# Performance work log

Hardware: AMD Instinct MI355X
Metric: run time of the kernel (lower is better)

Reference implementation:

```python
import jax, jax.numpy as jnp
import numpy as np

L, B, E, H = 2048, 4, 1024, 8
D1 = 2 * E  # expand_ratio * embed_dim, already divisible by H
EPS = 1e-8


def setup_inputs() -> dict:
    key = jax.random.key(0)
    ks = jax.random.split(key, 12)
    std = 0.02
    return {
        "query": jax.random.normal(ks[0], (L, B, E), jnp.float32),
        "key": jax.random.normal(ks[1], (L, B, E), jnp.float32),
        "value": jax.random.normal(ks[2], (L, B, E), jnp.float32),
        "u_w": jax.random.normal(ks[3], (D1, E), jnp.float32) * std,
        "u_b": jax.random.normal(ks[4], (D1,), jnp.float32) * std,
        "v_w": jax.random.normal(ks[5], (D1, E), jnp.float32) * std,
        "v_b": jax.random.normal(ks[6], (D1,), jnp.float32) * std,
        "o_w": jax.random.normal(ks[7], (E, D1), jnp.float32) * std,
        "o_b": jax.random.normal(ks[8], (E,), jnp.float32) * std,
        # Toeplitz relative-position coefficients: t_0 (zero), t_1..t_{n-1} (pos), t_{-1}..t_{-(n-1)} (neg)
        "pos": jax.random.normal(ks[9], (H, L - 1), jnp.float32) * std,
        "zero": jax.random.normal(ks[10], (H, 1), jnp.float32) * std,
        "neg": jax.random.normal(ks[11], (H, L - 1), jnp.float32) * std,
    }


def _toeplitz_mix(v, pos, zero, neg):
    # v: (b, h, n, d). y_i = sum_j t_{i-j} v_j via circular conv of length 2n.
    b, h, n, d = v.shape
    m = 2 * n
    # a[0]=t_0, a[1:n]=t_1..t_{n-1}, a[n]=0 (unused), a[n+1:2n]=t_{-(n-1)}..t_{-1}
    a = jnp.concatenate([zero, pos[:, : n - 1], jnp.zeros((h, 1), v.dtype), neg[:, : n - 1][:, ::-1]], axis=-1)
    af = jnp.fft.rfft(a, n=m, axis=-1)            # (h, n+1)
    vf = jnp.fft.rfft(v, n=m, axis=-2)            # (b, h, n+1, d)
    y = jnp.fft.irfft(af[None, :, :, None] * vf, n=m, axis=-2)
    return y[:, :, :n, :]


def reference(query, key, value, u_w, u_b, v_w, v_b, o_w, o_b, pos, zero, neg):
    n, b, e = query.shape
    # SimpleRMSNorm: x / (||x||_2 / sqrt(d) + eps)
    rms = jnp.linalg.norm(query, axis=-1, keepdims=True) * (e ** -0.5)
    x = query / (rms + EPS)
    u = jax.nn.silu(jnp.einsum("nbe,fe->nbf", x, u_w) + u_b)   # (n, b, d1)
    v = jax.nn.silu(jnp.einsum("nbe,fe->nbf", x, v_w) + v_b)   # (n, b, d1)
    hd = v.shape[-1] // H
    vh = v.reshape(n, b, H, hd).transpose(1, 2, 0, 3)          # (b, h, n, d)
    y = _toeplitz_mix(vh, pos, zero, neg)                      # (b, h, n, d)
    y = y.transpose(2, 0, 1, 3).reshape(n, b, H * hd)          # (n, b, d1)
    out = u * y
    return jnp.einsum("nbf,ef->nbe", out, o_w) + o_b + query
```

## Files before the change

kernel.cpp:

```cpp
#include <hip/hip_runtime.h>
#include <math.h>

typedef unsigned short u16;
typedef __bf16 bf16x8 __attribute__((ext_vector_type(8)));
typedef float f32x4 __attribute__((ext_vector_type(4)));

#define LSEQ 2048
#define NB   4
#define NE   1024
#define NHEAD 8
#define ND1  2048
#define NHD  256
#define NM   8192
#define CRP  4104

__device__ __forceinline__ u16 f2bf(float f) {
  unsigned u = __float_as_uint(f);
  u += 0x7FFFu + ((u >> 16) & 1u);
  return (u16)(u >> 16);
}
__device__ __forceinline__ float bf2f(u16 h) {
  return __uint_as_float(((unsigned)h) << 16);
}
__device__ __forceinline__ unsigned mulbf2(unsigned y2, unsigned u2) {
  float ylo = bf2f((u16)(y2 & 0xFFFF)), yhi = bf2f((u16)(y2 >> 16));
  float ulo = bf2f((u16)(u2 & 0xFFFF)), uhi = bf2f((u16)(u2 >> 16));
  return (unsigned)f2bf(ylo * ulo) | ((unsigned)f2bf(yhi * uhi) << 16);
}

__device__ __forceinline__ void gl_lds16(const u16* g, u16* l) {
  __builtin_amdgcn_global_load_lds(
      (const __attribute__((address_space(1))) void*)g,
      (__attribute__((address_space(3))) void*)l, 16, 0, 0);
}

__global__ __launch_bounds__(256) void prep_kernel(
    const float* __restrict__ uw, const float* __restrict__ vw,
    const float* __restrict__ ow, u16* __restrict__ uwb, u16* __restrict__ vwb,
    u16* __restrict__ owb, const float* __restrict__ pos,
    const float* __restrict__ zero, const float* __restrict__ neg,
    u16* __restrict__ cr8) {
  int bx = blockIdx.x;
  if (bx < 6144) {
    const float* s = bx < 2048 ? uw : (bx < 4096 ? vw : ow);
    u16* d = bx < 2048 ? uwb : (bx < 4096 ? vwb : owb);
    int i = (bx & 2047) * 256 + threadIdx.x;
    float4 v = ((const float4*)s)[i];
    ushort4 o;
    o.x = f2bf(v.x); o.y = f2bf(v.y); o.z = f2bf(v.z); o.w = f2bf(v.w);
    ((ushort4*)d)[i] = o;
  } else {
    int bb = bx - 6144;
    int h = bb >> 3, sh = bb & 7;
    u16* out = cr8 + (size_t)bb * CRP;
    for (int m = threadIdx.x; m < CRP; m += 256) {
      int mm = m + sh;
      float val = 0.f;
      if (mm <= 4094) {
        int t = 2047 - mm;
        if (t == 0)      val = zero[h];
        else if (t > 0)  val = pos[h * (LSEQ - 1) + t - 1];
        else             val = neg[h * (LSEQ - 1) + (-t) - 1];
      }
      out[m] = f2bf(val);
    }
  }
}

__global__ __launch_bounds__(256) void rmsnorm_kernel(const float* __restrict__ q,
                                                      u16* __restrict__ x) {
  int row = blockIdx.x;
  float4 v = ((const float4*)(q + (size_t)row * NE))[threadIdx.x];
  float ss = v.x * v.x + v.y * v.y + v.z * v.z + v.w * v.w;
  #pragma unroll
  for (int off = 32; off > 0; off >>= 1) ss += __shfl_down(ss, off, 64);
  __shared__ float wss[4];
  int wave = threadIdx.x >> 6, lane = threadIdx.x & 63;
  if (lane == 0) wss[wave] = ss;
  __syncthreads();
  float tot = wss[0] + wss[1] + wss[2] + wss[3];
  float scale = 1.f / (sqrtf(tot) * 0.03125f + 1e-8f);
  ushort4 o;
  o.x = f2bf(v.x * scale); o.y = f2bf(v.y * scale);
  o.z = f2bf(v.z * scale); o.w = f2bf(v.w * scale);
  ((ushort4*)(x + (size_t)row * NE))[threadIdx.x] = o;
}

__global__ __launch_bounds__(256) void transpose_v(const u16* __restrict__ v,
                                                   u16* __restrict__ vT) {
  __shared__ u16 s[64 * 68];
  int j0 = blockIdx.x * 64, d0 = blockIdx.y * 64;
  int h = blockIdx.z >> 2, b = blockIdx.z & 3;
  #pragma unroll
  for (int it = 0; it < 4; ++it) {
    int idx = it * 256 + threadIdx.x;
    int r = idx >> 4, c4 = idx & 15;
    *(ushort4*)&s[r * 68 + c4 * 4] =
        *(const ushort4*)&v[((size_t)(j0 + r) * NB + b) * ND1 + h * NHD + d0 + c4 * 4];
  }
  __syncthreads();
  #pragma unroll
  for (int it = 0; it < 4; ++it) {
    int idx = it * 256 + threadIdx.x;
    int cc = idx >> 4, jq = idx & 15;
    ushort4 o;
    o.x = s[(jq * 4 + 0) * 68 + cc];
    o.y = s[(jq * 4 + 1) * 68 + cc];
    o.z = s[(jq * 4 + 2) * 68 + cc];
    o.w = s[(jq * 4 + 3) * 68 + cc];
    *(ushort4*)&vT[((size_t)h * (NB * NHD) + b * NHD + d0 + cc) * LSEQ + j0 + jq * 4] = o;
  }
}


__device__ __forceinline__ bf16x8 ldsfrag(const u16* buf, int rr, int q) {
  return *(const bf16x8*)(buf + rr * 64 + ((q ^ (rr & 7)) * 8));
}

template <int MODE>
__device__ __forceinline__ void stage_Ah(const u16* A, const u16* Acr, int Ksz,
                                         int i0, int kt, int half, u16* dstbuf,
                                         int tid) {
  int wave = tid >> 6;
  #pragma unroll
  for (int it = 0; it < 2; ++it) {
    int vv = it * 512 + tid;
    int r = vv >> 3, c8 = vv & 7, c8s = c8 ^ (r & 7);
    int row = i0 + half * 128 + r;
    const u16* src;
    if (MODE != 1) {
      src = A + (size_t)row * Ksz + kt * 64 + c8s * 8;
    } else {
      int p = 2047 - row + kt * 64;
      int s = p & 7, qq = p - s;
      src = Acr + (size_t)s * CRP + qq + c8s * 8;
    }
    gl_lds16(src, dstbuf + half * 8192 + (it * 512 + wave * 64) * 8);
  }
}

__device__ __forceinline__ void stage_Bh(const u16* B, int Ksz, int n0, int kt,
                                         int half, u16* dstbuf, int tid) {
  int wave = tid >> 6;
  #pragma unroll
  for (int it = 0; it < 2; ++it) {
    int vv = it * 512 + tid;
    int r = vv >> 3, c8 = vv & 7, c8s = c8 ^ (r & 7);
    gl_lds16(B + (size_t)(n0 + half * 128 + r) * Ksz + kt * 64 + c8s * 8,
             dstbuf + half * 8192 + (it * 512 + wave * 64) * 8);
  }
}

#define PHASE_MID()                                        \
  __builtin_amdgcn_s_barrier();                            \
  asm volatile("s_waitcnt lgkmcnt(0)" ::: "memory");       \
  __builtin_amdgcn_sched_barrier(0);                       \
  __builtin_amdgcn_s_setprio(1);

#define PHASE_END()                                        \
  __builtin_amdgcn_s_setprio(0);                           \
  __builtin_amdgcn_s_barrier();                            \
  __builtin_amdgcn_sched_barrier(0);

template <int MODE>
__global__ __launch_bounds__(512, 2) void gemm256(
    const u16* __restrict__ A, const u16* __restrict__ Bw0,
    const u16* __restrict__ Bw1, const float* __restrict__ bias0,
    const float* __restrict__ bias1, u16* __restrict__ C0,
    u16* __restrict__ C1, int Msz, int Nsz, int Ksz) {
  extern __shared__ __align__(16) u16 lds[];
  u16* As = lds;
  u16* Ws = lds + 32768;

  const int tid = threadIdx.x;
  const int lane = tid & 63, wave = tid >> 6;
  const int wr = (wave >> 2) * 128, wc = (wave & 3) * 64;
  const int lr = lane & 15, lq = lane >> 4;
  const int i0 = blockIdx.y * 256, n0 = blockIdx.x * 256;

  const u16* Bh;
  const u16* Acr = A;
  const float* bias = bias0;
  u16* Cp = C0;
  if (MODE == 0) {
    Bh = blockIdx.z ? Bw1 : Bw0;
    bias = blockIdx.z ? bias1 : bias0;
    Cp = blockIdx.z ? C1 : C0;
  } else {
    Bh  = Bw0 + (size_t)blockIdx.z * Nsz * Ksz;
    Acr = A + (size_t)blockIdx.z * 8 * CRP;
  }
  const int nkt = Ksz >> 6;

  f32x4 acc[8][4];
  #pragma unroll
  for (int a = 0; a < 8; ++a)
    #pragma unroll
    for (int b = 0; b < 4; ++b) acc[a][b] = (f32x4){0.f, 0.f, 0.f, 0.f};

  stage_Ah<MODE>(A, Acr, Ksz, i0, 0, 0, As, tid);
  stage_Ah<MODE>(A, Acr, Ksz, i0, 0, 1, As, tid);
  stage_Bh(Bh, Ksz, n0, 0, 0, Ws, tid);
  stage_Bh(Bh, Ksz, n0, 0, 1, Ws, tid);
  stage_Bh(Bh, Ksz, n0, 1, 0, Ws + 16384, tid);
  stage_Bh(Bh, Ksz, n0, 1, 1, Ws + 16384, tid);
  asm volatile("s_waitcnt vmcnt(4)" ::: "memory");
  __builtin_amdgcn_s_barrier();
  __builtin_amdgcn_sched_barrier(0);

  for (int tt = 0; tt < nkt; ++tt) {
    const int cur = tt & 1;
    const u16* Ab = As + cur * 16384;
    const u16* Wb = Ws + cur * 16384;
    u16* An = As + (cur ^ 1) * 16384;
    u16* Wn = Ws + cur * 16384;

    bf16x8 a[4][2], b[4][2];

    #pragma unroll
    for (int rt = 0; rt < 4; ++rt) {
      int ar = wr + rt * 16 + lr;
      a[rt][0] = ldsfrag(Ab, ar, lq);
      a[rt][1] = ldsfrag(Ab, ar, 4 + lq);
    }
    #pragma unroll
    for (int ct = 0; ct < 4; ++ct) {
      int br = wc + ct * 16 + lr;
      b[ct][0] = ldsfrag(Wb, br, lq);
      b[ct][1] = ldsfrag(Wb, br, 4 + lq);
    }
    if (tt + 1 < nkt) {
      stage_Ah<MODE>(A, Acr, Ksz, i0, tt + 1, 0, An, tid);
      stage_Ah<MODE>(A, Acr, Ksz, i0, tt + 1, 1, An, tid);
    }
    PHASE_MID();
    #pragma unroll
    for (int rt = 0; rt < 4; ++rt)
      #pragma unroll
      for (int ct = 0; ct < 4; ++ct) {
        acc[rt][ct] = __builtin_amdgcn_mfma_f32_16x16x32_bf16(a[rt][0], b[ct][0], acc[rt][ct], 0, 0, 0);
        acc[rt][ct] = __builtin_amdgcn_mfma_f32_16x16x32_bf16(a[rt][1], b[ct][1], acc[rt][ct], 0, 0, 0);
      }
    PHASE_END();

    #pragma unroll
    for (int rt = 0; rt < 4; ++rt) {
      int ar = wr + (rt + 4) * 16 + lr;
      a[rt][0] = ldsfrag(Ab, ar, lq);
      a[rt][1] = ldsfrag(Ab, ar, 4 + lq);
    }
    if (tt + 2 < nkt) {
      stage_Bh(Bh, Ksz, n0, tt + 2, 0, Wn, tid);
      stage_Bh(Bh, Ksz, n0, tt + 2, 1, Wn, tid);
    }
    if (tt == nkt - 2) { asm volatile("s_waitcnt vmcnt(0)" ::: "memory"); }
    else               { asm volatile("s_waitcnt vmcnt(4)" ::: "memory"); }
    PHASE_MID();
    #pragma unroll
    for (int rt = 0; rt < 4; ++rt)
      #pragma unroll
      for (int ct = 0; ct < 4; ++ct) {
        acc[rt + 4][ct] = __builtin_amdgcn_mfma_f32_16x16x32_bf16(a[rt][0], b[ct][0], acc[rt + 4][ct], 0, 0, 0);
        acc[rt + 4][ct] = __builtin_amdgcn_mfma_f32_16x16x32_bf16(a[rt][1], b[ct][1], acc[rt + 4][ct], 0, 0, 0);
      }
    PHASE_END();
  }

  __syncthreads();
  u16* zl = lds;
  #pragma unroll
  for (int rt = 0; rt < 8; ++rt) {
    #pragma unroll
    for (int ct = 0; ct < 4; ++ct) {
      int col_l = wc + ct * 16 + lr;
      #pragma unroll
      for (int reg = 0; reg < 4; ++reg) {
        int row_l = wr + rt * 16 + lq * 4 + reg;
        float yv = acc[rt][ct][reg];
        if (MODE == 0) {
          float t = yv + bias[n0 + col_l];
          yv = t / (1.f + __expf(-t));
        }
        zl[row_l * 256 + (col_l ^ (((row_l >> 2) & 3) << 4))] = f2bf(yv);
      }
    }
  }
  __syncthreads();
  #pragma unroll
  for (int k = 0; k < 16; ++k) {
    int cc = k * 512 + tid;
    int row_l = cc >> 5, c8 = cc & 31;
    int colbase = c8 * 8;
    int swz = colbase ^ (((row_l >> 2) & 3) << 4);
    uint4 y4 = *(uint4*)&zl[row_l * 256 + swz];
    if (MODE == 0) {
      *(uint4*)&Cp[(size_t)(i0 + row_l) * Nsz + n0 + colbase] = y4;
    } else {
      size_t ui = ((size_t)(i0 + row_l) * NB + blockIdx.x) * ND1 +
                  (size_t)blockIdx.z * NHD + colbase;
      uint4 u4 = *(const uint4*)&Cp[ui];
      uint4 o;
      o.x = mulbf2(y4.x, u4.x); o.y = mulbf2(y4.y, u4.y);
      o.z = mulbf2(y4.z, u4.z); o.w = mulbf2(y4.w, u4.w);
      *(uint4*)&Cp[ui] = o;
    }
  }
}

__global__ __launch_bounds__(256) void gemm_out(
    const u16* __restrict__ A, const u16* __restrict__ Bw,
    const float* __restrict__ bias, const float* __restrict__ resid,
    float* __restrict__ Cf, int Nsz, int Ksz) {
  __shared__ __align__(16) u16 As[128 * 64];
  __shared__ __align__(16) u16 Ws[128 * 64];

  const int tid = threadIdx.x;
  const int lane = tid & 63, wave = tid >> 6;
  const int wr = (wave >> 1) * 64, wc = (wave & 1) * 64;
  const int lr = lane & 15, lq = lane >> 4;
  const int i0 = blockIdx.y * 128, n0 = blockIdx.x * 128;

  f32x4 acc[4][4];
  #pragma unroll
  for (int a = 0; a < 4; ++a)
    #pragma unroll
    for (int b = 0; b < 4; ++b) acc[a][b] = (f32x4){0.f, 0.f, 0.f, 0.f};

  const int nkt = Ksz >> 6;
  for (int kt = 0; kt < nkt; ++kt) {
    #pragma unroll
    for (int it = 0; it < 4; ++it) {
      int vv = tid + 256 * it;
      int r = vv >> 3, c8 = vv & 7;
      int c8s = c8 ^ (r & 7);
      gl_lds16(A + (size_t)(i0 + r) * Ksz + kt * 64 + c8s * 8,
               &As[(size_t)(wave * 64 + it * 256) * 8]);
    }
    #pragma unroll
    for (int it = 0; it < 4; ++it) {
      int vv = tid + 256 * it;
      int r = vv >> 3, c8 = vv & 7;
      int c8s = c8 ^ (r & 7);
      gl_lds16(Bw + (size_t)(n0 + r) * Ksz + kt * 64 + c8s * 8,
               &Ws[(size_t)(wave * 64 + it * 256) * 8]);
    }
    __syncthreads();
    #pragma unroll
    for (int ks = 0; ks < 2; ++ks) {
      bf16x8 af[4], bfr[4];
      #pragma unroll
      for (int rt = 0; rt < 4; ++rt) {
        int ar = wr + rt * 16 + lr;
        int cq = (ks * 4 + lq) ^ (ar & 7);
        af[rt] = *(const bf16x8*)&As[ar * 64 + cq * 8];
      }
      #pragma unroll
      for (int ct = 0; ct < 4; ++ct) {
        int br = wc + ct * 16 + lr;
        int cq = (ks * 4 + lq) ^ (br & 7);
        bfr[ct] = *(const bf16x8*)&Ws[br * 64 + cq * 8];
      }
      #pragma unroll
      for (int rt = 0; rt < 4; ++rt)
        #pragma unroll
        for (int ct = 0; ct < 4; ++ct)
          acc[rt][ct] = __builtin_amdgcn_mfma_f32_16x16x32_bf16(
              af[rt], bfr[ct], acc[rt][ct], 0, 0, 0);
    }
    __syncthreads();
  }

  #pragma unroll
  for (int rt = 0; rt < 4; ++rt) {
    #pragma unroll
    for (int ct = 0; ct < 4; ++ct) {
      int col = n0 + wc + ct * 16 + lr;
      #pragma unroll
      for (int reg = 0; reg < 4; ++reg) {
        int row = i0 + wr + rt * 16 + lq * 4 + reg;
        size_t oi = (size_t)row * Nsz + col;
        Cf[oi] = acc[rt][ct][reg] + bias[col] + resid[oi];
      }
    }
  }
}

extern "C" void kernel_launch(void* const* d_in, const int* in_sizes, int n_in,
                              void* d_out, int out_size, void* d_ws, size_t ws_size,
                              hipStream_t stream) {
  const float* q    = (const float*)d_in[0];
  const float* uw   = (const float*)d_in[3];
  const float* ub   = (const float*)d_in[4];
  const float* vw   = (const float*)d_in[5];
  const float* vb   = (const float*)d_in[6];
  const float* ow   = (const float*)d_in[7];
  const float* ob   = (const float*)d_in[8];
  const float* pos  = (const float*)d_in[9];
  const float* zero = (const float*)d_in[10];
  const float* neg  = (const float*)d_in[11];
  float* out = (float*)d_out;

  char* ws = (char*)d_ws;
  u16* x   = (u16*)(ws + 0);
  u16* uwb = (u16*)(ws + 16777216);
  u16* vwb = (u16*)(ws + 20971520);
  u16* owb = (u16*)(ws + 25165824);
  u16* u   = (u16*)(ws + 29360128);
  u16* v   = (u16*)(ws + 62914560);
  u16* vT  = (u16*)(ws + 96468992);
  u16* cr8 = (u16*)(ws + 130023424);

  hipFuncSetAttribute((const void*)gemm256<0>,
                      hipFuncAttributeMaxDynamicSharedMemorySize, 131072);
  hipFuncSetAttribute((const void*)gemm256<1>,
                      hipFuncAttributeMaxDynamicSharedMemorySize, 131072);

  prep_kernel<<<6208, 256, 0, stream>>>(uw, vw, ow, uwb, vwb, owb,
                                        pos, zero, neg, cr8);
  rmsnorm_kernel<<<NM, 256, 0, stream>>>(q, x);

  gemm256<0><<<dim3(8, 32, 2), 512, 131072, stream>>>(x, uwb, vwb, ub, vb, u, v,
                                                      NM, ND1, NE);
  transpose_v<<<dim3(32, 4, 32), 256, 0, stream>>>(v, vT);
  gemm256<1><<<dim3(4, 8, 8), 512, 131072, stream>>>(cr8, vT, nullptr, nullptr,
                                                     nullptr, u, nullptr,
                                                     LSEQ, NB * NHD, LSEQ);
  gemm_out<<<dim3(8, 64, 1), 256, 0, stream>>>(u, owb, ob, q, out, NE, ND1);
}
```

Measured before the change: 368.5 us.

## Fuse v transpose into projection GEMM epilogue, triple-buffer A, remap workgroups

Removes the separate transpose_v kernel: the v-projection blocks of the first GEMM now write their SiLU output transposed through LDS straight into the head-major vT layout. This drops one full write and read of the v intermediate and one kernel launch. The A operand staging goes from double to triple buffering with a deeper prefetch, raising dynamic LDS from 128 KB to 160 KB per block, which may lower the number of resident blocks per CU. Both GEMM kernels also remap workgroup IDs with a stride-8 interleave, intended to spread blocks across XCDs for better L2 locality.

```diff
diff --git a/kernel.cpp b/kernel.cpp
--- a/kernel.cpp
+++ b/kernel.cpp
@@ -86,32 +86,6 @@
   ((ushort4*)(x + (size_t)row * NE))[threadIdx.x] = o;
 }
 
-__global__ __launch_bounds__(256) void transpose_v(const u16* __restrict__ v,
-                                                   u16* __restrict__ vT) {
-  __shared__ u16 s[64 * 68];
-  int j0 = blockIdx.x * 64, d0 = blockIdx.y * 64;
-  int h = blockIdx.z >> 2, b = blockIdx.z & 3;
-  #pragma unroll
-  for (int it = 0; it < 4; ++it) {
-    int idx = it * 256 + threadIdx.x;
-    int r = idx >> 4, c4 = idx & 15;
-    *(ushort4*)&s[r * 68 + c4 * 4] =
-        *(const ushort4*)&v[((size_t)(j0 + r) * NB + b) * ND1 + h * NHD + d0 + c4 * 4];
-  }
-  __syncthreads();
-  #pragma unroll
-  for (int it = 0; it < 4; ++it) {
-    int idx = it * 256 + threadIdx.x;
-    int cc = idx >> 4, jq = idx & 15;
-    ushort4 o;
-    o.x = s[(jq * 4 + 0) * 68 + cc];
-    o.y = s[(jq * 4 + 1) * 68 + cc];
-    o.z = s[(jq * 4 + 2) * 68 + cc];
-    o.w = s[(jq * 4 + 3) * 68 + cc];
-    *(ushort4*)&vT[((size_t)h * (NB * NHD) + b * NHD + d0 + cc) * LSEQ + j0 + jq * 4] = o;
-  }
-}
-
 
 __device__ __forceinline__ bf16x8 ldsfrag(const u16* buf, int rr, int q) {
   return *(const bf16x8*)(buf + rr * 64 + ((q ^ (rr & 7)) * 8));
@@ -170,25 +144,32 @@
     u16* __restrict__ C1, int Msz, int Nsz, int Ksz) {
   extern __shared__ __align__(16) u16 lds[];
   u16* As = lds;
-  u16* Ws = lds + 32768;
+  u16* Ws = lds + 49152;
+
+  unsigned gx = gridDim.x, gy = gridDim.y;
+  unsigned nwg = gx * gy * gridDim.z;
+  unsigned lin = blockIdx.x + gx * (blockIdx.y + gy * blockIdx.z);
+  unsigned w = (lin & 7) * (nwg >> 3) + (lin >> 3);
+  unsigned bx = w % gx, rest = w / gx;
+  unsigned by = rest % gy, bz = rest / gy;
 
   const int tid = threadIdx.x;
   const int lane = tid & 63, wave = tid >> 6;
   const int wr = (wave >> 2) * 128, wc = (wave & 3) * 64;
   const int lr = lane & 15, lq = lane >> 4;
-  const int i0 = blockIdx.y * 256, n0 = blockIdx.x * 256;
+  const int i0 = by * 256, n0 = bx * 256;
 
   const u16* Bh;
   const u16* Acr = A;
   const float* bias = bias0;
   u16* Cp = C0;
   if (MODE == 0) {
-    Bh = blockIdx.z ? Bw1 : Bw0;
-    bias = blockIdx.z ? bias1 : bias0;
-    Cp = blockIdx.z ? C1 : C0;
+    Bh = bz ? Bw1 : Bw0;
+    bias = bz ? bias1 : bias0;
+    Cp = bz ? C1 : C0;
   } else {
-    Bh  = Bw0 + (size_t)blockIdx.z * Nsz * Ksz;
-    Acr = A + (size_t)blockIdx.z * 8 * CRP;
+    Bh  = Bw0 + (size_t)bz * Nsz * Ksz;
+    Acr = A + (size_t)bz * 8 * CRP;
   }
   const int nkt = Ksz >> 6;
 
@@ -202,18 +183,19 @@
   stage_Ah<MODE>(A, Acr, Ksz, i0, 0, 1, As, tid);
   stage_Bh(Bh, Ksz, n0, 0, 0, Ws, tid);
   stage_Bh(Bh, Ksz, n0, 0, 1, Ws, tid);
+  stage_Ah<MODE>(A, Acr, Ksz, i0, 1, 0, As + 16384, tid);
+  stage_Ah<MODE>(A, Acr, Ksz, i0, 1, 1, As + 16384, tid);
   stage_Bh(Bh, Ksz, n0, 1, 0, Ws + 16384, tid);
   stage_Bh(Bh, Ksz, n0, 1, 1, Ws + 16384, tid);
-  asm volatile("s_waitcnt vmcnt(4)" ::: "memory");
+  asm volatile("s_waitcnt vmcnt(8)" ::: "memory");
   __builtin_amdgcn_s_barrier();
   __builtin_amdgcn_sched_barrier(0);
 
   for (int tt = 0; tt < nkt; ++tt) {
-    const int cur = tt & 1;
-    const u16* Ab = As + cur * 16384;
-    const u16* Wb = Ws + cur * 16384;
-    u16* An = As + (cur ^ 1) * 16384;
-    u16* Wn = Ws + cur * 16384;
+    const u16* Ab = As + (tt % 3) * 16384;
+    const u16* Wb = Ws + (tt & 1) * 16384;
+    u16* An = As + ((tt + 2) % 3) * 16384;
+    u16* Wn = Ws + (tt & 1) * 16384;
 
     bf16x8 a[4][2], b[4][2];
 
@@ -229,9 +211,9 @@
       b[ct][0] = ldsfrag(Wb, br, lq);
       b[ct][1] = ldsfrag(Wb, br, 4 + lq);
     }
-    if (tt + 1 < nkt) {
-      stage_Ah<MODE>(A, Acr, Ksz, i0, tt + 1, 0, An, tid);
-      stage_Ah<MODE>(A, Acr, Ksz, i0, tt + 1, 1, An, tid);
+    if (tt + 2 < nkt) {
+      stage_Ah<MODE>(A, Acr, Ksz, i0, tt + 2, 0, An, tid);
+      stage_Ah<MODE>(A, Acr, Ksz, i0, tt + 2, 1, An, tid);
     }
     PHASE_MID();
     #pragma unroll
@@ -254,7 +236,7 @@
       stage_Bh(Bh, Ksz, n0, tt + 2, 1, Wn, tid);
     }
     if (tt == nkt - 2) { asm volatile("s_waitcnt vmcnt(0)" ::: "memory"); }
-    else               { asm volatile("s_waitcnt vmcnt(4)" ::: "memory"); }
+    else               { asm volatile("s_waitcnt vmcnt(8)" ::: "memory"); }
     PHASE_MID();
     #pragma unroll
     for (int rt = 0; rt < 4; ++rt)
@@ -267,6 +249,38 @@
   }
 
   __syncthreads();
+  if (MODE == 0 && bz == 1) {
+    u16* zt = lds;
+    #pragma unroll
+    for (int rt = 0; rt < 8; ++rt) {
+      #pragma unroll
+      for (int ct = 0; ct < 4; ++ct) {
+        int col_l = wc + ct * 16 + lr;
+        #pragma unroll
+        for (int reg = 0; reg < 4; ++reg) {
+          int row_l = wr + rt * 16 + lq * 4 + reg;
+          float t = acc[rt][ct][reg] + bias[n0 + col_l];
+          t = t / (1.f + __expf(-t));
+          zt[col_l * 256 + (row_l ^ (row_l >> 4) ^ ((col_l & 15) << 2))] = f2bf(t);
+        }
+      }
+    }
+    __syncthreads();
+    int j0 = by * 64;
+    #pragma unroll
+    for (int it2 = 0; it2 < 32; ++it2) {
+      int g = it2 * 512 + tid;
+      int jq = g & 15, b2 = (g >> 4) & 3, d = g >> 6;
+      int rl0 = 16 * jq + b2, sd = (d & 15) << 2;
+      ushort4 o;
+      o.x = zt[d * 256 + ((rl0 + 0)  ^ ((rl0 + 0)  >> 4) ^ sd)];
+      o.y = zt[d * 256 + ((rl0 + 4)  ^ ((rl0 + 4)  >> 4) ^ sd)];
+      o.z = zt[d * 256 + ((rl0 + 8)  ^ ((rl0 + 8)  >> 4) ^ sd)];
+      o.w = zt[d * 256 + ((rl0 + 12) ^ ((rl0 + 12) >> 4) ^ sd)];
+      *(ushort4*)&Cp[((size_t)bx * (NB * NHD) + b2 * NHD + d) * LSEQ + j0 + jq * 4] = o;
+    }
+    return;
+  }
   u16* zl = lds;
   #pragma unroll
   for (int rt = 0; rt < 8; ++rt) {
@@ -296,8 +310,8 @@
     if (MODE == 0) {
       *(uint4*)&Cp[(size_t)(i0 + row_l) * Nsz + n0 + colbase] = y4;
     } else {
-      size_t ui = ((size_t)(i0 + row_l) * NB + blockIdx.x) * ND1 +
-                  (size_t)blockIdx.z * NHD + colbase;
+      size_t ui = ((size_t)(i0 + row_l) * NB + bx) * ND1 +
+                  (size_t)bz * NHD + colbase;
       uint4 u4 = *(const uint4*)&Cp[ui];
       uint4 o;
       o.x = mulbf2(y4.x, u4.x); o.y = mulbf2(y4.y, u4.y);
@@ -314,11 +328,17 @@
   __shared__ __align__(16) u16 As[128 * 64];
   __shared__ __align__(16) u16 Ws[128 * 64];
 
+  unsigned gx = gridDim.x, gy = gridDim.y;
+  unsigned nwg = gx * gy;
+  unsigned lin = blockIdx.x + gx * blockIdx.y;
+  unsigned w = (lin & 7) * (nwg >> 3) + (lin >> 3);
+  unsigned bx = w % gx, by = w / gx;
+
   const int tid = threadIdx.x;
   const int lane = tid & 63, wave = tid >> 6;
   const int wr = (wave >> 1) * 64, wc = (wave & 1) * 64;
   const int lr = lane & 15, lq = lane >> 4;
-  const int i0 = blockIdx.y * 128, n0 = blockIdx.x * 128;
+  const int i0 = by * 128, n0 = bx * 128;
 
   f32x4 acc[4][4];
   #pragma unroll
@@ -406,23 +426,21 @@
   u16* vwb = (u16*)(ws + 20971520);
   u16* owb = (u16*)(ws + 25165824);
   u16* u   = (u16*)(ws + 29360128);
-  u16* v   = (u16*)(ws + 62914560);
   u16* vT  = (u16*)(ws + 96468992);
   u16* cr8 = (u16*)(ws + 130023424);
 
   hipFuncSetAttribute((const void*)gemm256<0>,
-                      hipFuncAttributeMaxDynamicSharedMemorySize, 131072);
+                      hipFuncAttributeMaxDynamicSharedMemorySize, 163840);
   hipFuncSetAttribute((const void*)gemm256<1>,
-                      hipFuncAttributeMaxDynamicSharedMemorySize, 131072);
+                      hipFuncAttributeMaxDynamicSharedMemorySize, 163840);
 
   prep_kernel<<<6208, 256, 0, stream>>>(uw, vw, ow, uwb, vwb, owb,
                                         pos, zero, neg, cr8);
   rmsnorm_kernel<<<NM, 256, 0, stream>>>(q, x);
 
-  gemm256<0><<<dim3(8, 32, 2), 512, 131072, stream>>>(x, uwb, vwb, ub, vb, u, v,
+  gemm256<0><<<dim3(8, 32, 2), 512, 163840, stream>>>(x, uwb, vwb, ub, vb, u, vT,
                                                       NM, ND1, NE);
-  transpose_v<<<dim3(32, 4, 32), 256, 0, stream>>>(v, vT);
-  gemm256<1><<<dim3(4, 8, 8), 512, 131072, stream>>>(cr8, vT, nullptr, nullptr,
+  gemm256<1><<<dim3(4, 8, 8), 512, 163840, stream>>>(cr8, vT, nullptr, nullptr,
                                                      nullptr, u, nullptr,
                                                      LSEQ, NB * NHD, LSEQ);
   gemm_out<<<dim3(8, 64, 1), 256, 0, stream>>>(u, owb, ob, q, out, NE, ND1);
```

Result: no change. 361.4 us (-1.9%).
